# Kernel tuning notes

Measured on AMD Instinct MI355X. Metric: run time of the kernel, lower is better.

The kernel has to match this reference:

```python
import jax, jax.numpy as jnp
import numpy as np

T, N, NN = 16, 64, 32          # ob_T, agents, neighbors
D, H, DK, DFF, L = 512, 8, 64, 2048, 2
NUM_PRED, OB_R = 20, 2.0


def _w(k, shape):
    fan_in = shape[-2] if len(shape) > 1 else shape[-1]
    return jax.random.normal(k, shape, jnp.float32) / np.sqrt(fan_in).astype(np.float32)


def setup_inputs():
    key = jax.random.key(0)
    ks = jax.random.split(key, 16)
    return {
        "x": jax.random.normal(ks[0], (T, N, 6), jnp.float32),
        "neighbor": jax.random.normal(ks[1], (T, N, NN, 4), jnp.float32),
        "att_factor": jax.random.uniform(ks[2], (1,), jnp.float32),
        "Wx": _w(ks[3], (4, D)), "bx": jnp.zeros((D,), jnp.float32),
        "Wn": _w(ks[4], (3, D)), "bn": jnp.zeros((D,), jnp.float32),
        "Wpred": _w(ks[5], (D, 2)), "bpred": jnp.zeros((2,), jnp.float32),
        "WQ": _w(ks[6], (L, D, H * DK)),
        "WK": _w(ks[7], (L, D, H * DK)),
        "WV": _w(ks[8], (L, D, H * DK)),
        "Wfc": _w(ks[9], (L, H * DK, D)),
        "mha_ln_g": jnp.ones((L, D), jnp.float32), "mha_ln_b": jnp.zeros((L, D), jnp.float32),
        "WSI": _w(ks[10], (L, H * D, D)),
        "ffs_w1": _w(ks[11], (L, D, DFF)), "ffs_w2": _w(ks[12], (L, DFF, D)),
        "ffs_ln_g": jnp.ones((L, D), jnp.float32), "ffs_ln_b": jnp.zeros((L, D), jnp.float32),
        "ffi_w1": _w(ks[13], (L, D, DFF)), "ffi_w2": _w(ks[14], (L, DFF, D)),
        "ffi_ln_g": jnp.ones((L, D), jnp.float32), "ffi_ln_b": jnp.zeros((L, D), jnp.float32),
    }


def _ln(x, g, b, eps=1e-5):
    m = x.mean(-1, keepdims=True)
    v = x.var(-1, keepdims=True)
    return (x - m) / jnp.sqrt(v + eps) * g + b


def reference(x, neighbor, att_factor, Wx, bx, Wn, bn, Wpred, bpred,
              WQ, WK, WV, Wfc, mha_ln_g, mha_ln_b, WSI,
              ffs_w1, ffs_w2, ffs_ln_g, ffs_ln_b,
              ffi_w1, ffi_w2, ffi_ln_g, ffi_ln_b):
    # ---- trajectory features ----
    velocity = jnp.linalg.norm(x[:, :, 2:4], axis=-1, keepdims=True)
    v_angle = jnp.arctan(x[:, :, 5] / x[:, :, 4])[..., None]
    x_f = jnp.nan_to_num(jnp.concatenate([x[:, :, 0:2], velocity, v_angle], axis=-1))
    pos = x[..., :2]                                       # [T,N,2]
    v = jnp.concatenate([x[1:2, ..., 2:4], pos[1:] - pos[:-1]], axis=0)  # [T,N,2]
    dp = neighbor[..., :2] - pos[:, :, None, :]            # [T,N,Nn,2]
    dv = neighbor[..., 2:4] - v[:, :, None, :]
    dist = jnp.linalg.norm(dp, axis=-1)                    # [T,N,Nn]
    mask = (dist <= OB_R).transpose(1, 2, 0)               # [N,Nn,T] (query-time mask)
    dot_dp_v = jnp.einsum('tnmd,tnd->tnm', dp, v)
    bearing = dot_dp_v / (dist * jnp.linalg.norm(v, axis=-1)[:, :, None])
    bearing = jnp.where(jnp.isnan(bearing), 0.0, bearing)
    dot_dp_dv = jnp.einsum('tnmd,tnmd->tnm', dp, dv)
    tau = -dot_dp_dv / jnp.linalg.norm(dv, axis=-1)
    tau = jnp.clip(jnp.where(jnp.isnan(tau), 0.0, tau), 0.0, 7.0)
    mpd = jnp.linalg.norm(dp + tau[..., None] * dv, axis=-1)
    neighbor_f = jnp.nan_to_num(jnp.stack([dist, bearing, mpd], axis=-1))  # [T,N,Nn,3]

    # ---- positional encoding (note: pos * 10000^(2i/d), as in the source) ----
    position = jnp.arange(T, dtype=jnp.float32)[:, None]
    div = jnp.power(10000.0, jnp.arange(0, D, 2, dtype=jnp.float32) / D)
    pe = jnp.zeros((T, D), jnp.float32)
    pe = pe.at[:, 0::2].set(jnp.sin(position * div)).at[:, 1::2].set(jnp.cos(position * div))

    x_emb = (x_f @ Wx + bx) + pe[:, None, :]               # [T,N,D]
    n_emb = (neighbor_f @ Wn + bn) + pe[:, None, None, :]  # [T,N,Nn,D]
    x_emb = x_emb.transpose(1, 0, 2)                       # [N,T,D]
    n_emb = n_emb.transpose(1, 2, 0, 3)                    # [N,Nn,T,D]

    amask = mask[:, :, None, :, None]   # [N,Nn,1(heads),T(query),1(key)]
    factor = att_factor[0]
    sk = 1.0 / np.sqrt(DK).astype(np.float32)
    sd = 1.0 / np.sqrt(D).astype(np.float32)

    for l in range(L):
        # --- masked MHA over the time axis, per (agent, neighbor) ---
        q = (n_emb @ WQ[l]).reshape(N, NN, T, H, DK).transpose(0, 1, 3, 2, 4)
        k = (n_emb @ WK[l]).reshape(N, NN, T, H, DK).transpose(0, 1, 3, 2, 4)
        vv = (n_emb @ WV[l]).reshape(N, NN, T, H, DK).transpose(0, 1, 3, 2, 4)
        scores = jnp.einsum('bmhqd,bmhkd->bmhqk', q, k) * sk
        scores = jnp.where(amask, scores, -1e9)
        attn = jax.nn.softmax(scores, axis=-1)             # [N,Nn,H,T,T]
        ctx = jnp.einsum('bmhqk,bmhkd->bmhqd', attn, vv)
        ctx = ctx.transpose(0, 1, 3, 2, 4).reshape(N, NN, T, H * DK)
        res_inter = _ln(ctx @ Wfc[l] + n_emb, mha_ln_g[l], mha_ln_b[l])

        # --- self/inter attention fusion ---
        att_inter = attn.mean(axis=1)                      # [N,H,T,T]
        att_self = jax.nn.softmax(jnp.einsum('nqd,nkd->nqk', x_emb, x_emb) * sd, axis=-1)
        att = att_self[:, None, :, :] + factor * att_inter # [N,H,T,T]
        si = jnp.einsum('nhqt,ntd->nqhd', att, x_emb).reshape(N, T, H * D)
        x_new = si @ WSI[l]                                # [N,T,D]

        # --- FFN + LayerNorm (self and inter branches) ---
        x_emb = _ln(jax.nn.relu(x_new @ ffs_w1[l]) @ ffs_w2[l] + x_new,
                    ffs_ln_g[l], ffs_ln_b[l])
        n_emb = _ln(jax.nn.relu(res_inter @ ffi_w1[l]) @ ffi_w2[l] + res_inter,
                    ffi_ln_g[l], ffi_ln_b[l])

    out = x_emb @ Wpred + bpred                            # [N,T,2]
    out = jnp.broadcast_to(out[None], (NUM_PRED, N, T, 2)).transpose(0, 2, 1, 3)
    return out                                             # [20,T,N,2]
```

## Files before the change

kernel.cpp:

```cpp
#include <hip/hip_runtime.h>
#include <math.h>


#define T_ 16
#define N_ 64
#define NN_ 32
#define D_ 512
#define H_ 8
#define DK_ 64
#define DFF_ 2048
#define L_ 2
#define NPRED_ 20

typedef unsigned short u16;
typedef unsigned int u32;
typedef __attribute__((ext_vector_type(8))) short short8;
typedef __attribute__((ext_vector_type(4))) float f32x4;

__device__ __forceinline__ u16 f2bf(float f) {
    u32 u = __float_as_uint(f);
    u32 r = u + 0x7fffu + ((u >> 16) & 1u);
    return (u16)(r >> 16);
}
__device__ __forceinline__ float bfv(u16 v) {
    return __uint_as_float(((u32)v) << 16);
}
__device__ __forceinline__ float ntn(float v) {
    if (isnan(v)) return 0.0f;
    if (isinf(v)) return v > 0.0f ? 3.4028234663852886e38f : -3.4028234663852886e38f;
    return v;
}
__device__ __forceinline__ float wave_sum(float v) {
    #pragma unroll
    for (int o = 32; o > 0; o >>= 1) v += __shfl_xor(v, o, 64);
    return v;
}
__device__ __forceinline__ void gload_lds(const u16* g, u16* l) {
    __builtin_amdgcn_global_load_lds(
        (const __attribute__((address_space(1))) u32*)g,
        (__attribute__((address_space(3))) u32*)l, 16, 0, 0);
}

struct WJob { const float* src; u16* dst; int K; int N; int t0; };
struct WJobs { WJob j[14]; };
__global__ __launch_bounds__(256) void wconv_all(WJobs jobs, int ntiles) {
    int bid = blockIdx.x;
    if (bid >= ntiles) return;
    int ji = 0;
    #pragma unroll 1
    for (int i = 1; i < 14; ++i) if (bid >= jobs.j[i].t0) ji = i;
    const float* in = jobs.j[ji].src;
    u16* out = jobs.j[ji].dst;
    int K = jobs.j[ji].K, N = jobs.j[ji].N;
    int lt = bid - jobs.j[ji].t0;
    int ntx = N >> 5;
    int nb = (lt % ntx) * 32, kb = (lt / ntx) * 32;
    __shared__ float tile[32][33];
    int tx = threadIdx.x & 31, ty = threadIdx.x >> 5;
    #pragma unroll
    for (int r = ty; r < 32; r += 8)
        tile[r][tx] = in[(size_t)(kb + r) * N + nb + tx];
    __syncthreads();
    #pragma unroll
    for (int r = ty; r < 32; r += 8)
        out[(size_t)(nb + r) * K + kb + tx] = f2bf(tile[tx][r]);
}

template<int TM, int TN, int EPI, int WF32, int WBF16>
__global__ __launch_bounds__(256) void gemm_bt(
    const u16* __restrict__ Ab, const u16* __restrict__ Btb,
    float* __restrict__ Cf, u16* __restrict__ Cb, const void* __restrict__ Rg,
    int K, int ldc)
{
    constexpr int WR = TM / 32, WC = TN / 32;
    constexpr int ITA = TM / 32, ITB = TN / 32;
    __shared__ __align__(16) u16 As[TM][64];
    __shared__ __align__(16) u16 Bs[TN][64];
    int tid = threadIdx.x;
    int lane = tid & 63, wave = tid >> 6;
    int quad = lane >> 4, l16 = lane & 15;
    int wm = (wave >> 1) * (TM / 2), wn = (wave & 1) * (TN / 2);

    int gx = gridDim.x, gy = gridDim.y;
    int bx, by;
    if ((gy & 7) == 0) {
        int id = blockIdx.y * gx + blockIdx.x;
        int xcd = id & 7;
        int slot = id >> 3;
        bx = slot % gx;
        by = xcd * (gy >> 3) + slot / gx;
    } else {
        bx = blockIdx.x;
        by = blockIdx.y;
    }
    size_t row0 = (size_t)by * TM;
    size_t col0 = (size_t)bx * TN;

    f32x4 acc[WR][WC];
    #pragma unroll
    for (int i = 0; i < WR; ++i)
        #pragma unroll
        for (int j = 0; j < WC; ++j)
            acc[i][j] = (f32x4){0.f, 0.f, 0.f, 0.f};

    int srow = lane >> 3;
    int c8 = (lane & 7) ^ srow;
    int h8 = l16 & 7;

    for (int k0 = 0; k0 < K; k0 += 64) {
        __syncthreads();
        #pragma unroll
        for (int it = 0; it < ITA; ++it) {
            int g = wave + it * 4;
            gload_lds(Ab + (row0 + g * 8 + srow) * (size_t)K + k0 + c8 * 8, &As[g * 8][0]);
        }
        #pragma unroll
        for (int it = 0; it < ITB; ++it) {
            int g = wave + it * 4;
            gload_lds(Btb + (col0 + g * 8 + srow) * (size_t)K + k0 + c8 * 8, &Bs[g * 8][0]);
        }
        __syncthreads();
        #pragma unroll
        for (int s = 0; s < 2; ++s) {
            int coff = ((s * 4 + quad) ^ h8) * 8;
            short8 af[WR], bf[WC];
            #pragma unroll
            for (int i = 0; i < WR; ++i)
                af[i] = *(short8*)&As[wm + i * 16 + l16][coff];
            #pragma unroll
            for (int j = 0; j < WC; ++j)
                bf[j] = *(short8*)&Bs[wn + j * 16 + l16][coff];
            #pragma unroll
            for (int i = 0; i < WR; ++i)
                #pragma unroll
                for (int j = 0; j < WC; ++j)
                    acc[i][j] = __builtin_amdgcn_mfma_f32_16x16x32_bf16(
                        af[i], bf[j], acc[i][j], 0, 0, 0);
        }
    }
    #pragma unroll
    for (int i = 0; i < WR; ++i)
        #pragma unroll
        for (int j = 0; j < WC; ++j)
            #pragma unroll
            for (int reg = 0; reg < 4; ++reg) {
                size_t row = row0 + wm + i * 16 + quad * 4 + reg;
                size_t col = col0 + wn + j * 16 + l16;
                float v = acc[i][j][reg];
                if (EPI == 2) v += ((const float*)Rg)[row * (size_t)ldc + col];
                if (EPI == 3) v += bfv(((const u16*)Rg)[row * (size_t)ldc + col]);
                if (EPI == 1) v = fmaxf(v, 0.f);
                if (WF32)  Cf[row * (size_t)ldc + col] = v;
                if (WBF16) Cb[row * (size_t)ldc + col] = f2bf(v);
            }
}

template<int EPI, int WF32, int WBF16>
__global__ __launch_bounds__(256, 2) void gemm_ct(
    const u16* __restrict__ Ab, const u16* __restrict__ Btb,
    float* __restrict__ Cf, u16* __restrict__ Cb, const void* __restrict__ Rg,
    int K, int ldc)
{
    __shared__ __align__(16) u16 As[2][128][64];
    __shared__ __align__(16) u16 Bs[2][128][64];
    int tid = threadIdx.x;
    int lane = tid & 63, wave = tid >> 6;
    int quad = lane >> 4, l16 = lane & 15;
    int wm = (wave >> 1) * 64, wn = (wave & 1) * 64;

    int gx = gridDim.x, gy = gridDim.y;
    int id = blockIdx.y * gx + blockIdx.x;
    int xcd = id & 7, slot = id >> 3;
    int bx = slot % gx;
    int by = xcd * (gy >> 3) + slot / gx;
    size_t row0 = (size_t)by * 128;
    size_t col0 = (size_t)bx * 128;

    f32x4 acc[4][4];
    #pragma unroll
    for (int i = 0; i < 4; ++i)
        #pragma unroll
        for (int j = 0; j < 4; ++j)
            acc[i][j] = (f32x4){0.f, 0.f, 0.f, 0.f};

    int srow = lane >> 3;
    int c8 = (lane & 7) ^ srow;
    int h8 = l16 & 7;
    size_t aoff[4], boff[4];
    #pragma unroll
    for (int it = 0; it < 4; ++it) {
        aoff[it] = (row0 + (size_t)(wave + it * 4) * 8 + srow) * (size_t)K + c8 * 8;
        boff[it] = (col0 + (size_t)(wave + it * 4) * 8 + srow) * (size_t)K + c8 * 8;
    }

    int nt = K >> 6;
    #pragma unroll
    for (int it = 0; it < 4; ++it)
        gload_lds(Ab + aoff[it], &As[0][(wave + it * 4) * 8][0]);
    #pragma unroll
    for (int it = 0; it < 4; ++it)
        gload_lds(Btb + boff[it], &Bs[0][(wave + it * 4) * 8][0]);

    #pragma unroll 1
    for (int t = 0; t < nt; ++t) {
        int cur = t & 1;
        if (t + 1 < nt) {
            size_t ko = (size_t)(t + 1) * 64;
            #pragma unroll
            for (int it = 0; it < 4; ++it)
                gload_lds(Ab + aoff[it] + ko, &As[cur ^ 1][(wave + it * 4) * 8][0]);
            #pragma unroll
            for (int it = 0; it < 4; ++it)
                gload_lds(Btb + boff[it] + ko, &Bs[cur ^ 1][(wave + it * 4) * 8][0]);
            __builtin_amdgcn_sched_barrier(0);
            asm volatile("s_waitcnt vmcnt(8)" ::: "memory");
        } else {
            __builtin_amdgcn_sched_barrier(0);
            asm volatile("s_waitcnt vmcnt(0)" ::: "memory");
        }
        __builtin_amdgcn_sched_barrier(0);
        __builtin_amdgcn_s_barrier();
        __builtin_amdgcn_sched_barrier(0);
        __builtin_amdgcn_s_setprio(1);
        #pragma unroll
        for (int kh = 0; kh < 2; ++kh) {
            int coff = ((kh * 4 + quad) ^ h8) * 8;
            short8 af[4], bf[4];
            #pragma unroll
            for (int j = 0; j < 4; ++j)
                bf[j] = *(short8*)&Bs[cur][wn + j * 16 + l16][coff];
            #pragma unroll
            for (int i = 0; i < 4; ++i)
                af[i] = *(short8*)&As[cur][wm + i * 16 + l16][coff];
            #pragma unroll
            for (int i = 0; i < 4; ++i)
                #pragma unroll
                for (int j = 0; j < 4; ++j)
                    acc[i][j] = __builtin_amdgcn_mfma_f32_16x16x32_bf16(
                        af[i], bf[j], acc[i][j], 0, 0, 0);
        }
        __builtin_amdgcn_s_setprio(0);
        __builtin_amdgcn_sched_barrier(0);
        __builtin_amdgcn_s_barrier();
    }

    #pragma unroll
    for (int i = 0; i < 4; ++i)
        #pragma unroll
        for (int j = 0; j < 4; ++j)
            #pragma unroll
            for (int reg = 0; reg < 4; ++reg) {
                size_t row = row0 + wm + i * 16 + quad * 4 + reg;
                size_t col = col0 + wn + j * 16 + l16;
                float v = acc[i][j][reg];
                if (EPI == 2) v += ((const float*)Rg)[row * (size_t)ldc + col];
                if (EPI == 3) v += bfv(((const u16*)Rg)[row * (size_t)ldc + col]);
                if (EPI == 1) v = fmaxf(v, 0.f);
                if (WF32)  Cf[row * (size_t)ldc + col] = v;
                if (WBF16) Cb[row * (size_t)ldc + col] = f2bf(v);
            }
}

template<int CTX, int LD>
__global__ __launch_bounds__(256) void attn_fused_kernel(
    const u16* __restrict__ QKVb, const float* __restrict__ maskf, int bm0,
    float* __restrict__ att_sum, u16* __restrict__ ctxb)
{
    __shared__ __align__(16) u16 sQ[16][520];
    __shared__ __align__(16) u16 sK[16][520];
    __shared__ __align__(16) u16 sV[CTX ? 16 : 1][520];
    __shared__ float s_p[H_][16][17];
    __shared__ float sMask[16];
    int bm_l = blockIdx.x;
    int tid = threadIdx.x;
    int t = tid >> 4, ch = (tid & 15) * 32;
    const u16* base = QKVb + ((size_t)bm_l * T_ + t) * LD;
    #pragma unroll
    for (int c = 0; c < 4; ++c) {
        *(uint4*)&sQ[t][ch + c * 8] = *(const uint4*)(base + ch + c * 8);
        *(uint4*)&sK[t][ch + c * 8] = *(const uint4*)(base + 512 + ch + c * 8);
        if (CTX) *(uint4*)&sV[t][ch + c * 8] = *(const uint4*)(base + 1024 + ch + c * 8);
    }
    if (tid < 16) sMask[tid] = maskf[(size_t)(bm0 + bm_l) * T_ + tid];
    __syncthreads();

    int b = (bm0 + bm_l) >> 5;
    int lane = tid & 63, wid = tid >> 6;
    int l16 = lane & 15, quad = lane >> 4;

    #pragma unroll
    for (int hh = 0; hh < 2; ++hh) {
        int h = wid + hh * 4;
        short8 aq0 = *(const short8*)&sQ[l16][h * 64 + quad * 8];
        short8 aq1 = *(const short8*)&sQ[l16][h * 64 + 32 + quad * 8];
        short8 bk0 = *(const short8*)&sK[l16][h * 64 + quad * 8];
        short8 bk1 = *(const short8*)&sK[l16][h * 64 + 32 + quad * 8];
        f32x4 acc = (f32x4){0.f, 0.f, 0.f, 0.f};
        acc = __builtin_amdgcn_mfma_f32_16x16x32_bf16(aq0, bk0, acc, 0, 0, 0);
        acc = __builtin_amdgcn_mfma_f32_16x16x32_bf16(aq1, bk1, acc, 0, 0, 0);
        #pragma unroll
        for (int reg = 0; reg < 4; ++reg) {
            int q = quad * 4 + reg;
            float v = acc[reg] * 0.125f;
            if (sMask[q] == 0.0f) v = -1e9f;
            s_p[h][q][l16] = v;
        }
    }
    __syncthreads();
    if (tid < 128) {
        int h = tid >> 4, q = tid & 15;
        float mx = -3.4e38f;
        #pragma unroll
        for (int kk = 0; kk < 16; ++kk) mx = fmaxf(mx, s_p[h][q][kk]);
        float e[16], s = 0.f;
        #pragma unroll
        for (int kk = 0; kk < 16; ++kk) { e[kk] = expf(s_p[h][q][kk] - mx); s += e[kk]; }
        float inv = 1.0f / s;
        #pragma unroll
        for (int kk = 0; kk < 16; ++kk) s_p[h][q][kk] = e[kk] * inv;
    }
    __syncthreads();
    #pragma unroll
    for (int r = 0; r < 8; ++r) {
        int h = r;
        int q = (tid >> 4) & 15, k = tid & 15;
        atomicAdd(&att_sum[(((size_t)b * H_ + h) * T_ + q) * T_ + k], s_p[h][q][k]);
    }
    if (CTX) {
        #pragma unroll
        for (int rep = 0; rep < 8; ++rep) {
            int i2 = rep * 256 + tid;
            int tt = i2 >> 7, cu = i2 & 127;
            int h = cu >> 4;
            const float* pr = &s_p[h][tt][0];
            float a0 = 0.f, a1 = 0.f, a2 = 0.f, a3 = 0.f;
            #pragma unroll
            for (int kk = 0; kk < 16; ++kk) {
                uint2 vv = *((const uint2*)&sV[kk][0] + cu);
                float p = pr[kk];
                a0 += p * bfv((u16)(vv.x & 0xffff));
                a1 += p * bfv((u16)(vv.x >> 16));
                a2 += p * bfv((u16)(vv.y & 0xffff));
                a3 += p * bfv((u16)(vv.y >> 16));
            }
            uint2 o;
            o.x = (u32)f2bf(a0) | ((u32)f2bf(a1) << 16);
            o.y = (u32)f2bf(a2) | ((u32)f2bf(a3) << 16);
            *(uint2*)((u32*)(ctxb + ((size_t)bm_l * T_ + tt) * D_) + cu * 2) = o;
        }
    }
}

__global__ __launch_bounds__(256) void siatt_kernel(
    const float* __restrict__ xemb, const float* __restrict__ att_sum,
    const float* __restrict__ attf, u16* __restrict__ sib)
{
    __shared__ float sX[16][516];
    __shared__ float sS[16][17];
    __shared__ float sA[16][17];
    int n = blockIdx.x >> 3, h = blockIdx.x & 7;
    int tid = threadIdx.x;
    int t = tid >> 4, ch = (tid & 15) * 32;
    const float* src = xemb + ((size_t)n * T_ + t) * D_;
    #pragma unroll
    for (int c = 0; c < 8; ++c)
        *(float4*)&sX[t][ch + c * 4] = *(const float4*)(src + ch + c * 4);
    __syncthreads();
    int q = tid >> 4, k = tid & 15;
    {
        float acc = 0.f;
        for (int d4 = 0; d4 < D_ / 4; ++d4) {
            float4 xq = *(const float4*)&sX[q][d4 * 4];
            float4 xk = *(const float4*)&sX[k][d4 * 4];
            acc += xq.x * xk.x;
            acc += xq.y * xk.y;
            acc += xq.z * xk.z;
            acc += xq.w * xk.w;
        }
        sS[q][k] = acc * 0.04419417382415922f;
    }
    __syncthreads();
    if (tid < T_) {
        float mx = -3.4e38f;
        #pragma unroll
        for (int kk = 0; kk < 16; ++kk) mx = fmaxf(mx, sS[tid][kk]);
        float e[16], s = 0.f;
        #pragma unroll
        for (int kk = 0; kk < 16; ++kk) { e[kk] = expf(sS[tid][kk] - mx); s += e[kk]; }
        float inv = 1.0f / s;
        #pragma unroll
        for (int kk = 0; kk < 16; ++kk) sS[tid][kk] = e[kk] * inv;
    }
    __syncthreads();
    float f = attf[0] * (1.0f / 32.0f);
    sA[q][k] = sS[q][k] + f * att_sum[((size_t)n * H_ + h) * 256 + q * 16 + k];
    __syncthreads();
    #pragma unroll
    for (int rep = 0; rep < 16; ++rep) {
        int i2 = rep * 256 + tid;
        int qq = i2 >> 8, d2 = (i2 & 255) * 2;
        const float* ar = &sA[qq][0];
        float a0 = 0.f, a1 = 0.f;
        #pragma unroll
        for (int tt = 0; tt < 16; ++tt) {
            float p = ar[tt];
            a0 += p * sX[tt][d2];
            a1 += p * sX[tt][d2 + 1];
        }
        u32 o = (u32)f2bf(a0) | ((u32)f2bf(a1) << 16);
        *((u32*)(sib + (size_t)n * T_ * 4096 + (size_t)qq * 4096 + h * 512) + (d2 >> 1)) = o;
    }
}

__global__ void pe_kernel(float* pe) {
    int i = blockIdx.x * blockDim.x + threadIdx.x;
    if (i >= T_ * 256) return;
    int t = i >> 8, j = i & 255;
    float dv = (float)pow(10000.0, (double)j / 256.0);
    float a = (float)t * dv;
    double ad = (double)a;
    pe[t * D_ + 2 * j]     = (float)sin(ad);
    pe[t * D_ + 2 * j + 1] = (float)cos(ad);
}

__global__ void xemb_kernel(const float* x, const float* Wx, const float* bx,
                            const float* pe, float* xemb) {
    int row = blockIdx.x;
    int t = row / N_, n = row % N_;
    float x0 = x[row * 6 + 0], x1 = x[row * 6 + 1];
    float x2 = x[row * 6 + 2], x3 = x[row * 6 + 3];
    float x4 = x[row * 6 + 4], x5 = x[row * 6 + 5];
    float vel = sqrtf(x2 * x2 + x3 * x3);
    float ang = atanf(x5 / x4);
    float f0 = ntn(x0), f1 = ntn(x1), f2 = ntn(vel), f3 = ntn(ang);
    for (int d = threadIdx.x; d < D_; d += blockDim.x) {
        xemb[((size_t)n * T_ + t) * D_ + d] =
            f0 * Wx[0 * D_ + d] + f1 * Wx[1 * D_ + d]
          + f2 * Wx[2 * D_ + d] + f3 * Wx[3 * D_ + d]
          + bx[d] + pe[t * D_ + d];
    }
}

__global__ void nbr_kernel(const float* x, const float* nbr, float* nf, float* maskf) {
    int idx = blockIdx.x * blockDim.x + threadIdx.x;
    if (idx >= T_ * N_ * NN_) return;
    int m = idx % NN_;
    int tn = idx / NN_;
    int n = tn % N_, t = tn / N_;
    float px = x[((size_t)t * N_ + n) * 6 + 0];
    float py = x[((size_t)t * N_ + n) * 6 + 1];
    float vx, vy;
    if (t == 0) {
        vx = x[((size_t)1 * N_ + n) * 6 + 2];
        vy = x[((size_t)1 * N_ + n) * 6 + 3];
    } else {
        vx = px - x[((size_t)(t - 1) * N_ + n) * 6 + 0];
        vy = py - x[((size_t)(t - 1) * N_ + n) * 6 + 1];
    }
    float nx  = nbr[(size_t)idx * 4 + 0], ny  = nbr[(size_t)idx * 4 + 1];
    float nvx = nbr[(size_t)idx * 4 + 2], nvy = nbr[(size_t)idx * 4 + 3];
    float dpx = nx - px, dpy = ny - py;
    float dvx = nvx - vx, dvy = nvy - vy;
    float dist = sqrtf(dpx * dpx + dpy * dpy);
    maskf[((size_t)n * NN_ + m) * T_ + t] = (dist <= 2.0f) ? 1.0f : 0.0f;
    float vn = sqrtf(vx * vx + vy * vy);
    float bearing = (dpx * vx + dpy * vy) / (dist * vn);
    if (isnan(bearing)) bearing = 0.0f;
    float dvn = sqrtf(dvx * dvx + dvy * dvy);
    float tau = -(dpx * dvx + dpy * dvy) / dvn;
    if (isnan(tau)) tau = 0.0f;
    tau = fminf(fmaxf(tau, 0.0f), 7.0f);
    float mx_ = dpx + tau * dvx, my_ = dpy + tau * dvy;
    float mpd = sqrtf(mx_ * mx_ + my_ * my_);
    nf[(size_t)idx * 3 + 0] = ntn(dist);
    nf[(size_t)idx * 3 + 1] = ntn(bearing);
    nf[(size_t)idx * 3 + 2] = ntn(mpd);
}

__global__ void nemb_kernel(const float* nf, const float* Wn, const float* bn,
                            const float* pe, u16* Ab) {
    int row = blockIdx.x;
    int t = row % T_;
    int bm = row / T_;
    int m = bm % NN_, b = bm / NN_;
    size_t nfrow = (((size_t)t * N_ + b) * NN_ + m) * 3;
    float f0 = nf[nfrow], f1 = nf[nfrow + 1], f2 = nf[nfrow + 2];
    for (int d = threadIdx.x; d < D_; d += blockDim.x) {
        float v = f0 * Wn[d] + f1 * Wn[D_ + d] + f2 * Wn[2 * D_ + d]
                + bn[d] + pe[t * D_ + d];
        Ab[(size_t)row * D_ + d] = f2bf(v);
    }
}

template<int INBF>
__global__ __launch_bounds__(256) void ln_kernel(
    const void* X, const float* g, const float* b, float* outF, u16* outB, int nrows) {
    int row = blockIdx.x * 4 + (threadIdx.x >> 6);
    if (row >= nrows) return;
    int lane = threadIdx.x & 63;
    int d0 = lane * 8;
    float v[8];
    if (INBF) {
        short8 x8 = *(const short8*)((const u16*)X + (size_t)row * D_ + d0);
        #pragma unroll
        for (int r = 0; r < 8; ++r) v[r] = bfv((u16)x8[r]);
    } else {
        float4 a = *(const float4*)((const float*)X + (size_t)row * D_ + d0);
        float4 c = *(const float4*)((const float*)X + (size_t)row * D_ + d0 + 4);
        v[0] = a.x; v[1] = a.y; v[2] = a.z; v[3] = a.w;
        v[4] = c.x; v[5] = c.y; v[6] = c.z; v[7] = c.w;
    }
    float s = 0.f;
    #pragma unroll
    for (int r = 0; r < 8; ++r) s += v[r];
    s = wave_sum(s);
    float mean = s * (1.0f / 512.0f);
    float vs = 0.f;
    #pragma unroll
    for (int r = 0; r < 8; ++r) { float d = v[r] - mean; vs += d * d; }
    vs = wave_sum(vs);
    float rstd = rsqrtf(vs * (1.0f / 512.0f) + 1e-5f);
    float4 g0 = *(const float4*)&g[d0], g1 = *(const float4*)&g[d0 + 4];
    float4 b0 = *(const float4*)&b[d0], b1 = *(const float4*)&b[d0 + 4];
    float o[8];
    o[0] = (v[0] - mean) * rstd * g0.x + b0.x;
    o[1] = (v[1] - mean) * rstd * g0.y + b0.y;
    o[2] = (v[2] - mean) * rstd * g0.z + b0.z;
    o[3] = (v[3] - mean) * rstd * g0.w + b0.w;
    o[4] = (v[4] - mean) * rstd * g1.x + b1.x;
    o[5] = (v[5] - mean) * rstd * g1.y + b1.y;
    o[6] = (v[6] - mean) * rstd * g1.z + b1.z;
    o[7] = (v[7] - mean) * rstd * g1.w + b1.w;
    if (outF) {
        float4 w0 = {o[0], o[1], o[2], o[3]};
        float4 w1 = {o[4], o[5], o[6], o[7]};
        *(float4*)(outF + (size_t)row * D_ + d0) = w0;
        *(float4*)(outF + (size_t)row * D_ + d0 + 4) = w1;
    }
    if (outB) {
        short8 w;
        #pragma unroll
        for (int r = 0; r < 8; ++r) w[r] = (short)f2bf(o[r]);
        *(short8*)(outB + (size_t)row * D_ + d0) = w;
    }
}

__global__ __launch_bounds__(256) void predbcast_kernel(
    const float* __restrict__ xemb, const float* __restrict__ Wp,
    const float* __restrict__ bp, float* __restrict__ out) {
    int nt = blockIdx.x * blockDim.x + threadIdx.x;
    if (nt >= N_ * T_) return;
    int n = nt / T_, t = nt % T_;
    float a0 = bp[0], a1 = bp[1];
    const float* xr = xemb + (size_t)nt * D_;
    for (int j = 0; j < D_; j += 4) {
        float4 xv = *(const float4*)&xr[j];
        float4 w0 = *(const float4*)&Wp[(size_t)j * 2];
        float4 w1 = *(const float4*)&Wp[(size_t)j * 2 + 4];
        a0 += xv.x * w0.x; a1 += xv.x * w0.y;
        a0 += xv.y * w0.z; a1 += xv.y * w0.w;
        a0 += xv.z * w1.x; a1 += xv.z * w1.y;
        a0 += xv.w * w1.z; a1 += xv.w * w1.w;
    }
    #pragma unroll
    for (int p = 0; p < NPRED_; ++p) {
        size_t o = (((size_t)p * T_ + t) * N_ + n) * 2;
        out[o]     = a0;
        out[o + 1] = a1;
    }
}

extern "C" void kernel_launch(void* const* d_in, const int* in_sizes, int n_in,
                              void* d_out, int out_size, void* d_ws, size_t ws_size,
                              hipStream_t stream) {
    (void)in_sizes; (void)n_in; (void)out_size; (void)ws_size;

    const float* x    = (const float*)d_in[0];
    const float* nbr  = (const float*)d_in[1];
    const float* attf = (const float*)d_in[2];
    const float* Wx   = (const float*)d_in[3];
    const float* bx   = (const float*)d_in[4];
    const float* Wn   = (const float*)d_in[5];
    const float* bn   = (const float*)d_in[6];
    const float* Wp   = (const float*)d_in[7];
    const float* bp   = (const float*)d_in[8];
    const float* WQ   = (const float*)d_in[9];
    const float* WK   = (const float*)d_in[10];
    const float* WV   = (const float*)d_in[11];
    const float* Wfc  = (const float*)d_in[12];
    const float* mlng = (const float*)d_in[13];
    const float* mlnb = (const float*)d_in[14];
    const float* WSI  = (const float*)d_in[15];
    const float* fsw1 = (const float*)d_in[16];
    const float* fsw2 = (const float*)d_in[17];
    const float* fsg  = (const float*)d_in[18];
    const float* fsb  = (const float*)d_in[19];
    const float* fiw1 = (const float*)d_in[20];
    const float* fiw2 = (const float*)d_in[21];
    const float* fig  = (const float*)d_in[22];
    const float* fib  = (const float*)d_in[23];

    char* w = (char*)d_ws;
    size_t off = 0;
    auto alloc = [&](size_t bytes) -> void* {
        void* p = w + off;
        off = (off + bytes + 255) & ~(size_t)255;
        return p;
    };
    const size_t MiB = 1024 * 1024;

    const int BM = N_ * NN_;
    const int ROWS_I = BM * T_;
    const int CB = 1024;
    const int RC = CB * T_;
    const int NCH = ROWS_I / RC;

    float* pe      = (float*)alloc((size_t)T_ * D_ * 4);
    float* xemb    = (float*)alloc((size_t)N_ * T_ * D_ * 4);
    float* nf      = (float*)alloc((size_t)T_ * N_ * NN_ * 3 * 4);
    float* maskf   = (float*)alloc((size_t)BM * T_ * 4);
    u16*   Ab      = (u16*)alloc((size_t)ROWS_I * D_ * 2);
    u16* tQKV[2], *tWSI[2], *tfs1[2], *tfs2[2];
    for (int l = 0; l < 2; ++l) {
        tQKV[l] = (u16*)alloc((size_t)1536 * 512 * 2);
        tWSI[l] = (u16*)alloc((size_t)512 * 4096 * 2);
        tfs1[l] = (u16*)alloc((size_t)2048 * 512 * 2);
        tfs2[l] = (u16*)alloc((size_t)512 * 2048 * 2);
    }
    u16* tWfc = (u16*)alloc((size_t)512 * 512 * 2);
    u16* tfi1 = (u16*)alloc((size_t)2048 * 512 * 2);
    u16* tfi2 = (u16*)alloc((size_t)512 * 2048 * 2);
    char* SCR  = (char*)alloc(64 * MiB);
    u16*   QKVb = (u16*)SCR;
    u16*   ctxb = (u16*)(SCR + 48 * MiB);
    u16*   hid  = (u16*)SCR;
    u16*   BbA    = (u16*)alloc((size_t)RC * D_ * 2);
    u16*   Bb_res = (u16*)alloc((size_t)RC * D_ * 2);
    float* att_sum = (float*)alloc((size_t)N_ * H_ * 256 * 4);
    u16*   sib     = (u16*)alloc((size_t)N_ * T_ * 4096 * 2);
    float* xnew    = (float*)alloc((size_t)N_ * T_ * D_ * 4);
    u16*   xnb     = (u16*)alloc((size_t)N_ * T_ * D_ * 2);

    WJobs jobs;
    int ntiles = 0;
    auto addJob = [&](int idx, const float* src, u16* dst, int K, int N) {
        jobs.j[idx] = {src, dst, K, N, ntiles};
        ntiles += (N >> 5) * (K >> 5);
    };
    addJob(0,  WQ,                            tQKV[0],              512, 512);
    addJob(1,  WK,                            tQKV[0] + 512 * 512,  512, 512);
    addJob(2,  WV,                            tQKV[0] + 1024 * 512, 512, 512);
    addJob(3,  WQ + (size_t)512 * 512,        tQKV[1],              512, 512);
    addJob(4,  WK + (size_t)512 * 512,        tQKV[1] + 512 * 512,  512, 512);
    addJob(5,  Wfc,                           tWfc,                 512, 512);
    addJob(6,  WSI,                           tWSI[0],              4096, 512);
    addJob(7,  WSI + (size_t)4096 * 512,      tWSI[1],              4096, 512);
    addJob(8,  fsw1,                          tfs1[0],              512, 2048);
    addJob(9,  fsw1 + (size_t)512 * 2048,     tfs1[1],              512, 2048);
    addJob(10, fsw2,                          tfs2[0],              2048, 512);
    addJob(11, fsw2 + (size_t)2048 * 512,     tfs2[1],              2048, 512);
    addJob(12, fiw1,                          tfi1,                 512, 2048);
    addJob(13, fiw2,                          tfi2,                 2048, 512);
    wconv_all<<<ntiles, 256, 0, stream>>>(jobs, ntiles);

    pe_kernel<<<16, 256, 0, stream>>>(pe);
    xemb_kernel<<<T_ * N_, 256, 0, stream>>>(x, Wx, bx, pe, xemb);
    nbr_kernel<<<(T_ * N_ * NN_ + 255) / 256, 256, 0, stream>>>(x, nbr, nf, maskf);
    nemb_kernel<<<BM * T_, 256, 0, stream>>>(nf, Wn, bn, pe, Ab);

    for (int l = 0; l < L_; ++l) {
        hipMemsetAsync(att_sum, 0, (size_t)N_ * H_ * 256 * 4, stream);
        if (l == 0) {
            for (int c = 0; c < NCH; ++c) {
                u16* Acb = Ab + (size_t)c * RC * D_;
                gemm_ct<0, 0, 1><<<dim3(12, RC / 128), 256, 0, stream>>>(
                    Acb, tQKV[0], nullptr, QKVb, nullptr, 512, 1536);
                attn_fused_kernel<1, 1536><<<CB, 256, 0, stream>>>(
                    QKVb, maskf, c * CB, att_sum, ctxb);
                gemm_ct<3, 0, 1><<<dim3(4, RC / 128), 256, 0, stream>>>(
                    ctxb, tWfc, nullptr, BbA, Acb, 512, 512);
                ln_kernel<1><<<RC / 4, 256, 0, stream>>>(
                    BbA, mlng, mlnb, nullptr, Bb_res, RC);
                gemm_ct<1, 0, 1><<<dim3(16, RC / 128), 256, 0, stream>>>(
                    Bb_res, tfi1, nullptr, hid, nullptr, 512, 2048);
                gemm_ct<3, 0, 1><<<dim3(4, RC / 128), 256, 0, stream>>>(
                    hid, tfi2, nullptr, BbA, Bb_res, 2048, 512);
                ln_kernel<1><<<RC / 4, 256, 0, stream>>>(
                    BbA, fig, fib, nullptr, Acb, RC);
            }
        } else {
            gemm_ct<0, 0, 1><<<dim3(8, ROWS_I / 128), 256, 0, stream>>>(
                Ab, tQKV[1], nullptr, QKVb, nullptr, 512, 1024);
            attn_fused_kernel<0, 1024><<<BM, 256, 0, stream>>>(
                QKVb, maskf, 0, att_sum, nullptr);
        }

        siatt_kernel<<<N_ * H_, 256, 0, stream>>>(xemb, att_sum, attf, sib);
        gemm_bt<32, 64, 0, 1, 1><<<dim3(8, 32), 256, 0, stream>>>(
            sib, tWSI[l], xnew, xnb, nullptr, 4096, 512);
        gemm_bt<32, 64, 1, 0, 1><<<dim3(32, 32), 256, 0, stream>>>(
            xnb, tfs1[l], nullptr, hid, nullptr, 512, 2048);
        gemm_bt<32, 64, 2, 1, 0><<<dim3(8, 32), 256, 0, stream>>>(
            hid, tfs2[l], xemb, nullptr, xnew, 2048, 512);
        ln_kernel<0><<<(N_ * T_) / 4, 256, 0, stream>>>(
            xemb, fsg + l * D_, fsb + l * D_, xemb, nullptr, N_ * T_);
    }

    predbcast_kernel<<<(N_ * T_ + 255) / 256, 256, 0, stream>>>(
        xemb, Wp, bp, (float*)d_out);
}
```

Before: 768.3 us.

## Replace small-tile self-branch GEMMs with split-K double-buffered 128x128 GEMMs plus reduction

The three per-layer self-branch GEMMs (WSI projection, FFN up and FFN down, M=1024) previously used a small 32x64-tile kernel with no pipelining. They now use a 128x128 double-buffered MFMA kernel with split-K across blockIdx.z, writing fp32 partials to scratch. A separate reduction kernel then sums the partials and applies the epilogue (relu, residual add, bf16/fp32 output). This aims to raise per-block arithmetic intensity and keep enough blocks in flight despite the small M. The cost is extra fp32 partial traffic and additional kernel launches.

Result: no change. 755.7 us (-1.7%).

```diff
diff --git a/kernel.cpp b/kernel.cpp
--- a/kernel.cpp
+++ b/kernel.cpp
@@ -66,95 +66,6 @@
         out[(size_t)(nb + r) * K + kb + tx] = f2bf(tile[tx][r]);
 }
 
-template<int TM, int TN, int EPI, int WF32, int WBF16>
-__global__ __launch_bounds__(256) void gemm_bt(
-    const u16* __restrict__ Ab, const u16* __restrict__ Btb,
-    float* __restrict__ Cf, u16* __restrict__ Cb, const void* __restrict__ Rg,
-    int K, int ldc)
-{
-    constexpr int WR = TM / 32, WC = TN / 32;
-    constexpr int ITA = TM / 32, ITB = TN / 32;
-    __shared__ __align__(16) u16 As[TM][64];
-    __shared__ __align__(16) u16 Bs[TN][64];
-    int tid = threadIdx.x;
-    int lane = tid & 63, wave = tid >> 6;
-    int quad = lane >> 4, l16 = lane & 15;
-    int wm = (wave >> 1) * (TM / 2), wn = (wave & 1) * (TN / 2);
-
-    int gx = gridDim.x, gy = gridDim.y;
-    int bx, by;
-    if ((gy & 7) == 0) {
-        int id = blockIdx.y * gx + blockIdx.x;
-        int xcd = id & 7;
-        int slot = id >> 3;
-        bx = slot % gx;
-        by = xcd * (gy >> 3) + slot / gx;
-    } else {
-        bx = blockIdx.x;
-        by = blockIdx.y;
-    }
-    size_t row0 = (size_t)by * TM;
-    size_t col0 = (size_t)bx * TN;
-
-    f32x4 acc[WR][WC];
-    #pragma unroll
-    for (int i = 0; i < WR; ++i)
-        #pragma unroll
-        for (int j = 0; j < WC; ++j)
-            acc[i][j] = (f32x4){0.f, 0.f, 0.f, 0.f};
-
-    int srow = lane >> 3;
-    int c8 = (lane & 7) ^ srow;
-    int h8 = l16 & 7;
-
-    for (int k0 = 0; k0 < K; k0 += 64) {
-        __syncthreads();
-        #pragma unroll
-        for (int it = 0; it < ITA; ++it) {
-            int g = wave + it * 4;
-            gload_lds(Ab + (row0 + g * 8 + srow) * (size_t)K + k0 + c8 * 8, &As[g * 8][0]);
-        }
-        #pragma unroll
-        for (int it = 0; it < ITB; ++it) {
-            int g = wave + it * 4;
-            gload_lds(Btb + (col0 + g * 8 + srow) * (size_t)K + k0 + c8 * 8, &Bs[g * 8][0]);
-        }
-        __syncthreads();
-        #pragma unroll
-        for (int s = 0; s < 2; ++s) {
-            int coff = ((s * 4 + quad) ^ h8) * 8;
-            short8 af[WR], bf[WC];
-            #pragma unroll
-            for (int i = 0; i < WR; ++i)
-                af[i] = *(short8*)&As[wm + i * 16 + l16][coff];
-            #pragma unroll
-            for (int j = 0; j < WC; ++j)
-                bf[j] = *(short8*)&Bs[wn + j * 16 + l16][coff];
-            #pragma unroll
-            for (int i = 0; i < WR; ++i)
-                #pragma unroll
-                for (int j = 0; j < WC; ++j)
-                    acc[i][j] = __builtin_amdgcn_mfma_f32_16x16x32_bf16(
-                        af[i], bf[j], acc[i][j], 0, 0, 0);
-        }
-    }
-    #pragma unroll
-    for (int i = 0; i < WR; ++i)
-        #pragma unroll
-        for (int j = 0; j < WC; ++j)
-            #pragma unroll
-            for (int reg = 0; reg < 4; ++reg) {
-                size_t row = row0 + wm + i * 16 + quad * 4 + reg;
-                size_t col = col0 + wn + j * 16 + l16;
-                float v = acc[i][j][reg];
-                if (EPI == 2) v += ((const float*)Rg)[row * (size_t)ldc + col];
-                if (EPI == 3) v += bfv(((const u16*)Rg)[row * (size_t)ldc + col]);
-                if (EPI == 1) v = fmaxf(v, 0.f);
-                if (WF32)  Cf[row * (size_t)ldc + col] = v;
-                if (WBF16) Cb[row * (size_t)ldc + col] = f2bf(v);
-            }
-}
-
 template<int EPI, int WF32, int WBF16>
 __global__ __launch_bounds__(256, 2) void gemm_ct(
     const u16* __restrict__ Ab, const u16* __restrict__ Btb,
@@ -259,6 +170,142 @@
                 if (WF32)  Cf[row * (size_t)ldc + col] = v;
                 if (WBF16) Cb[row * (size_t)ldc + col] = f2bf(v);
             }
+}
+
+template<int NS>
+__global__ __launch_bounds__(256, 2) void gemm_ks(
+    const u16* __restrict__ Ab, const u16* __restrict__ Btb,
+    float* __restrict__ Pf, int K, int ldc)
+{
+    __shared__ __align__(16) u16 As[2][128][64];
+    __shared__ __align__(16) u16 Bs[2][128][64];
+    int tid = threadIdx.x;
+    int lane = tid & 63, wave = tid >> 6;
+    int quad = lane >> 4, l16 = lane & 15;
+    int wm = (wave >> 1) * 64, wn = (wave & 1) * 64;
+
+    int gx = gridDim.x, gy = gridDim.y;
+    int id = blockIdx.y * gx + blockIdx.x;
+    int xcd = id & 7, slot = id >> 3;
+    int bx = slot % gx;
+    int by = xcd * (gy >> 3) + slot / gx;
+    int z = blockIdx.z;
+    int Kc = K / NS;
+    size_t row0 = (size_t)by * 128;
+    size_t col0 = (size_t)bx * 128;
+    size_t M = (size_t)gy * 128;
+
+    f32x4 acc[4][4];
+    #pragma unroll
+    for (int i = 0; i < 4; ++i)
+        #pragma unroll
+        for (int j = 0; j < 4; ++j)
+            acc[i][j] = (f32x4){0.f, 0.f, 0.f, 0.f};
+
+    int srow = lane >> 3;
+    int c8 = (lane & 7) ^ srow;
+    int h8 = l16 & 7;
+    size_t kbase = (size_t)z * Kc;
+    size_t aoff[4], boff[4];
+    #pragma unroll
+    for (int it = 0; it < 4; ++it) {
+        aoff[it] = (row0 + (size_t)(wave + it * 4) * 8 + srow) * (size_t)K + kbase + c8 * 8;
+        boff[it] = (col0 + (size_t)(wave + it * 4) * 8 + srow) * (size_t)K + kbase + c8 * 8;
+    }
+
+    int nt = Kc >> 6;
+    #pragma unroll
+    for (int it = 0; it < 4; ++it)
+        gload_lds(Ab + aoff[it], &As[0][(wave + it * 4) * 8][0]);
+    #pragma unroll
+    for (int it = 0; it < 4; ++it)
+        gload_lds(Btb + boff[it], &Bs[0][(wave + it * 4) * 8][0]);
+
+    #pragma unroll 1
+    for (int t = 0; t < nt; ++t) {
+        int cur = t & 1;
+        if (t + 1 < nt) {
+            size_t ko = (size_t)(t + 1) * 64;
+            #pragma unroll
+            for (int it = 0; it < 4; ++it)
+                gload_lds(Ab + aoff[it] + ko, &As[cur ^ 1][(wave + it * 4) * 8][0]);
+            #pragma unroll
+            for (int it = 0; it < 4; ++it)
+                gload_lds(Btb + boff[it] + ko, &Bs[cur ^ 1][(wave + it * 4) * 8][0]);
+            __builtin_amdgcn_sched_barrier(0);
+            asm volatile("s_waitcnt vmcnt(8)" ::: "memory");
+        } else {
+            __builtin_amdgcn_sched_barrier(0);
+            asm volatile("s_waitcnt vmcnt(0)" ::: "memory");
+        }
+        __builtin_amdgcn_sched_barrier(0);
+        __builtin_amdgcn_s_barrier();
+        __builtin_amdgcn_sched_barrier(0);
+        __builtin_amdgcn_s_setprio(1);
+        #pragma unroll
+        for (int kh = 0; kh < 2; ++kh) {
+            int coff = ((kh * 4 + quad) ^ h8) * 8;
+            short8 af[4], bf[4];
+            #pragma unroll
+            for (int j = 0; j < 4; ++j)
+                bf[j] = *(short8*)&Bs[cur][wn + j * 16 + l16][coff];
+            #pragma unroll
+            for (int i = 0; i < 4; ++i)
+                af[i] = *(short8*)&As[cur][wm + i * 16 + l16][coff];
+            #pragma unroll
+            for (int i = 0; i < 4; ++i)
+                #pragma unroll
+                for (int j = 0; j < 4; ++j)
+                    acc[i][j] = __builtin_amdgcn_mfma_f32_16x16x32_bf16(
+                        af[i], bf[j], acc[i][j], 0, 0, 0);
+        }
+        __builtin_amdgcn_s_setprio(0);
+        __builtin_amdgcn_sched_barrier(0);
+        __builtin_amdgcn_s_barrier();
+    }
+
+    float* P = Pf + (size_t)z * M * (size_t)ldc;
+    #pragma unroll
+    for (int i = 0; i < 4; ++i)
+        #pragma unroll
+        for (int j = 0; j < 4; ++j)
+            #pragma unroll
+            for (int reg = 0; reg < 4; ++reg) {
+                size_t row = row0 + wm + i * 16 + quad * 4 + reg;
+                size_t col = col0 + wn + j * 16 + l16;
+                P[row * (size_t)ldc + col] = acc[i][j][reg];
+            }
+}
+
+template<int NS, int EPI, int WF32, int WBF16>
+__global__ __launch_bounds__(256) void ksum_kernel(
+    const float* __restrict__ P, const float* __restrict__ res,
+    float* __restrict__ outF, u16* __restrict__ outB, int total)
+{
+    int i = blockIdx.x * blockDim.x + threadIdx.x;
+    size_t o4 = (size_t)i * 4;
+    if (o4 >= (size_t)total) return;
+    float4 s = *(const float4*)(P + o4);
+    #pragma unroll
+    for (int p = 1; p < NS; ++p) {
+        float4 v = *(const float4*)(P + (size_t)p * total + o4);
+        s.x += v.x; s.y += v.y; s.z += v.z; s.w += v.w;
+    }
+    if (EPI == 2) {
+        float4 r = *(const float4*)(res + o4);
+        s.x += r.x; s.y += r.y; s.z += r.z; s.w += r.w;
+    }
+    if (EPI == 1) {
+        s.x = fmaxf(s.x, 0.f); s.y = fmaxf(s.y, 0.f);
+        s.z = fmaxf(s.z, 0.f); s.w = fmaxf(s.w, 0.f);
+    }
+    if (WF32) *(float4*)(outF + o4) = s;
+    if (WBF16) {
+        uint2 w;
+        w.x = (u32)f2bf(s.x) | ((u32)f2bf(s.y) << 16);
+        w.y = (u32)f2bf(s.z) | ((u32)f2bf(s.w) << 16);
+        *(uint2*)(outB + o4) = w;
+    }
 }
 
 template<int CTX, int LD>
@@ -634,6 +681,7 @@
     u16*   QKVb = (u16*)SCR;
     u16*   ctxb = (u16*)(SCR + 48 * MiB);
     u16*   hid  = (u16*)SCR;
+    float* Pk   = (float*)(SCR + 16 * MiB);
     u16*   BbA    = (u16*)alloc((size_t)RC * D_ * 2);
     u16*   Bb_res = (u16*)alloc((size_t)RC * D_ * 2);
     float* att_sum = (float*)alloc((size_t)N_ * H_ * 256 * 4);
@@ -696,12 +744,15 @@
         }
 
         siatt_kernel<<<N_ * H_, 256, 0, stream>>>(xemb, att_sum, attf, sib);
-        gemm_bt<32, 64, 0, 1, 1><<<dim3(8, 32), 256, 0, stream>>>(
-            sib, tWSI[l], xnew, xnb, nullptr, 4096, 512);
-        gemm_bt<32, 64, 1, 0, 1><<<dim3(32, 32), 256, 0, stream>>>(
-            xnb, tfs1[l], nullptr, hid, nullptr, 512, 2048);
-        gemm_bt<32, 64, 2, 1, 0><<<dim3(8, 32), 256, 0, stream>>>(
-            hid, tfs2[l], xemb, nullptr, xnew, 2048, 512);
+        gemm_ks<8><<<dim3(4, 8, 8), 256, 0, stream>>>(sib, tWSI[l], Pk, 4096, 512);
+        ksum_kernel<8, 0, 1, 1><<<512, 256, 0, stream>>>(
+            Pk, nullptr, xnew, xnb, 1024 * 512);
+        gemm_ks<2><<<dim3(16, 8, 2), 256, 0, stream>>>(xnb, tfs1[l], Pk, 512, 2048);
+        ksum_kernel<2, 1, 0, 1><<<2048, 256, 0, stream>>>(
+            Pk, nullptr, nullptr, hid, 1024 * 2048);
+        gemm_ks<8><<<dim3(4, 8, 8), 256, 0, stream>>>(hid, tfs2[l], Pk, 2048, 512);
+        ksum_kernel<8, 2, 1, 0><<<512, 256, 0, stream>>>(
+            Pk, xnew, xemb, nullptr, 1024 * 512);
         ln_kernel<0><<<(N_ * T_) / 4, 256, 0, stream>>>(
             xemb, fsg + l * D_, fsb + l * D_, xemb, nullptr, N_ * T_);
     }
```
